# Kernel optimization log

Hardware: AMD Instinct MI355X
Metric: run time of the kernel (lower is better)

## Reference

```python
import jax, jax.numpy as jnp
import numpy as np

HID = 64; D_INNER = 128; D_STATE = 16; DT_RANK = 4; GROUP = 3

def _ln(x, g, b, eps=1e-5):
    m = x.mean(-1, keepdims=True)
    v = ((x - m) ** 2).mean(-1, keepdims=True)
    return (x - m) * jax.lax.rsqrt(v + eps) * g + b

def _conv1x1(x, w, b):
    # x: (B,C,H,W), w: (O,C)
    return jnp.einsum('bchw,oc->bohw', x, w) + b[None, :, None, None]

def _pixel_exchange(F):
    # F: (3,B,C,H,W); vectorized row- then column-exchange with group_size==num_features==3
    _, B, C, H, W = F.shape
    rows = jnp.arange(H); cols = jnp.arange(W)
    R = []
    for d in range(GROUP):
        idx = (d + rows % GROUP) % GROUP  # source feature per row
        R.append(jnp.transpose(F[idx, :, :, rows, :], (1, 2, 0, 3)))
    Rs = jnp.stack(R)
    out = []
    for d in range(GROUP):
        jdx = (d + cols % GROUP) % GROUP  # source feature per column
        out.append(jnp.transpose(Rs[jdx, :, :, :, cols], (1, 2, 3, 0)))
    return out

def _selective_scan(xs, dts, Bs, Cs, A, D):
    # xs,dts: (B,4,d,L); Bs,Cs: (B,4,N,L); A: (4,d,N); D: (4,d)
    xs_t = jnp.moveaxis(xs, -1, 0); dts_t = jnp.moveaxis(dts, -1, 0)
    Bs_t = jnp.moveaxis(Bs, -1, 0); Cs_t = jnp.moveaxis(Cs, -1, 0)
    h0 = jnp.zeros((xs.shape[0], 4, D_INNER, D_STATE), xs.dtype)
    def step(h, inp):
        x_t, dt_t, B_t, C_t = inp
        dA = jnp.exp(dt_t[..., None] * A)
        h = dA * h + (dt_t * x_t)[..., None] * B_t[:, :, None, :]
        y = jnp.einsum('bkdn,bkn->bkd', h, C_t)
        return h, y
    _, ys = jax.lax.scan(step, h0, (xs_t, dts_t, Bs_t, Cs_t))
    ys = jnp.moveaxis(ys, 0, -1)  # (B,4,d,L)
    return ys + D[None, :, :, None] * xs

def _ss2d(x, in_w, in_b, conv_w, conv_b, xproj_w, dt_w, dt_b, A_log, Ds, onorm_g, onorm_b, out_w, out_b):
    B, H, W, C = x.shape; L = H * W
    xz = x @ in_w.T + in_b
    xc, z = xz[..., :D_INNER], xz[..., D_INNER:]
    xc = jnp.transpose(xc, (0, 3, 1, 2))  # (B,d,H,W)
    xc = jax.lax.conv_general_dilated(xc, conv_w, (1, 1), 'SAME',
        dimension_numbers=('NCHW', 'OIHW', 'NCHW'), feature_group_count=D_INNER) + conv_b[None, :, None, None]
    xc = jax.nn.silu(xc)
    x_hw = xc.reshape(B, D_INNER, L)
    x_wh = jnp.transpose(xc, (0, 1, 3, 2)).reshape(B, D_INNER, L)
    xs = jnp.stack([x_hw, x_wh, jnp.flip(x_hw, -1), jnp.flip(x_wh, -1)], axis=1)  # (B,4,d,L)
    x_dbl = jnp.einsum('bkdl,kcd->bkcl', xs, xproj_w)
    dts = jnp.einsum('bkrl,kdr->bkdl', x_dbl[:, :, :DT_RANK], dt_w) + dt_b[None, :, :, None]
    dts = jax.nn.softplus(dts)
    Bs = x_dbl[:, :, DT_RANK:DT_RANK + D_STATE]
    Cs = x_dbl[:, :, DT_RANK + D_STATE:]
    A = -jnp.exp(A_log)
    ys = _selective_scan(xs, dts, Bs, Cs, A, Ds)
    wh2hw = lambda y: jnp.transpose(y.reshape(B, D_INNER, W, H), (0, 1, 3, 2)).reshape(B, D_INNER, L)
    y = ys[:, 0] + jnp.flip(ys[:, 2], -1) + wh2hw(ys[:, 1]) + wh2hw(jnp.flip(ys[:, 3], -1))
    y = _ln(jnp.transpose(y, (0, 2, 1)), onorm_g, onorm_b)  # (B,L,d)
    y = y * jax.nn.silu(z.reshape(B, L, D_INNER))
    return (y @ out_w.T + out_b).reshape(B, H, W, HID)

def _vss(x, p):
    return x + _ss2d(_ln(x, p[0], p[1]), *p[2:])

def reference(x1, x2, x3, aw1, ab1, aw2, ab2, aw3, ab3, ln_g, ln_b, in_w, in_b, conv_w, conv_b, xproj_w, dt_w, dt_b, A_log, Ds, onorm_g, onorm_b, out_w, out_b, k1_w, k1_b, k2_w, k2_b, q3_w, q3_b, v3_w, v3_b, proj_w, proj_b, bn_g, bn_b):
    feats = jnp.stack([_conv1x1(x1, aw1, ab1), _conv1x1(x2, aw2, ab2), _conv1x1(x3, aw3, ab3)])
    ex = _pixel_exchange(feats)
    vss_out = []
    for i in range(3):
        p = (ln_g[i], ln_b[i], in_w[i], in_b[i], conv_w[i], conv_b[i], xproj_w[i], dt_w[i], dt_b[i], A_log[i], Ds[i], onorm_g[i], onorm_b[i], out_w[i], out_b[i])
        xin = jnp.transpose(ex[i], (0, 2, 3, 1))
        vss_out.append(jnp.transpose(_vss(xin, p), (0, 3, 1, 2)))
    v1, v2, v3 = vss_out
    B, C, H, W = v1.shape; L = H * W
    K1 = _conv1x1(v1, k1_w, k1_b).reshape(B, C, L)
    K2 = _conv1x1(v2, k2_w, k2_b).reshape(B, C, L)
    Q = jnp.transpose(_conv1x1(v3, q3_w, q3_b).reshape(B, C, L), (0, 2, 1))
    V = jnp.transpose(_conv1x1(v3, v3_w, v3_b).reshape(B, C, L), (0, 2, 1))
    scale = 1.0 / jnp.sqrt(jnp.asarray(C, jnp.float32))
    a1 = jax.nn.softmax(jnp.einsum('blc,bcm->blm', Q, K1) * scale, axis=-1)
    O1 = jnp.einsum('blm,bmc->blc', a1, V)
    a2 = jax.nn.softmax(jnp.einsum('blc,bcm->blm', Q, K2) * scale, axis=-1)
    O2 = jnp.einsum('blm,bmc->blc', a2, V)
    fused = jnp.transpose(O1 + O2, (0, 2, 1)).reshape(B, C, H, W)
    cat = jnp.concatenate([fused, v1, v2], axis=1)
    out = _conv1x1(cat, proj_w, proj_b)
    m = out.mean((0, 2, 3), keepdims=True)
    var = ((out - m) ** 2).mean((0, 2, 3), keepdims=True)
    out = (out - m) * jax.lax.rsqrt(var + 1e-5) * bn_g[None, :, None, None] + bn_b[None, :, None, None]
    return jax.nn.relu(out)

def setup_inputs() -> dict:
    key = jax.random.key(0)
    ks = iter(jax.random.split(key, 64))
    nrm = lambda shape, s=0.02: jax.random.normal(next(ks), shape, jnp.float32) * s
    B, H, W = 2, 64, 64
    d = {}
    d['x1'] = jax.random.normal(next(ks), (B, 128, H, W), jnp.float32)
    d['x2'] = jax.random.normal(next(ks), (B, 256, H, W), jnp.float32)
    d['x3'] = jax.random.normal(next(ks), (B, 512, H, W), jnp.float32)
    d['aw1'] = nrm((HID, 128)); d['ab1'] = jnp.zeros((HID,), jnp.float32)
    d['aw2'] = nrm((HID, 256)); d['ab2'] = jnp.zeros((HID,), jnp.float32)
    d['aw3'] = nrm((HID, 512)); d['ab3'] = jnp.zeros((HID,), jnp.float32)
    d['ln_g'] = jnp.ones((3, HID), jnp.float32); d['ln_b'] = jnp.zeros((3, HID), jnp.float32)
    d['in_w'] = nrm((3, 2 * D_INNER, HID)); d['in_b'] = jnp.zeros((3, 2 * D_INNER), jnp.float32)
    d['conv_w'] = nrm((3, D_INNER, 1, 3, 3), 0.1); d['conv_b'] = jnp.zeros((3, D_INNER), jnp.float32)
    d['xproj_w'] = nrm((3, 4, DT_RANK + 2 * D_STATE, D_INNER))
    d['dt_w'] = nrm((3, 4, D_INNER, DT_RANK), 0.1); d['dt_b'] = nrm((3, 4, D_INNER), 0.1)
    d['A_log'] = jnp.log(jnp.broadcast_to(jnp.arange(1, D_STATE + 1, dtype=jnp.float32), (3, 4, D_INNER, D_STATE)))
    d['Ds'] = jnp.ones((3, 4, D_INNER), jnp.float32)
    d['onorm_g'] = jnp.ones((3, D_INNER), jnp.float32); d['onorm_b'] = jnp.zeros((3, D_INNER), jnp.float32)
    d['out_w'] = nrm((3, HID, D_INNER)); d['out_b'] = jnp.zeros((3, HID), jnp.float32)
    for nm in ['k1', 'k2', 'q3', 'v3']:
        d[nm + '_w'] = nrm((HID, HID)); d[nm + '_b'] = jnp.zeros((HID,), jnp.float32)
    d['proj_w'] = nrm((HID, 3 * HID)); d['proj_b'] = jnp.zeros((HID,), jnp.float32)
    d['bn_g'] = jnp.ones((HID,), jnp.float32); d['bn_b'] = jnp.zeros((HID,), jnp.float32)
    return d
```

## Files before the change

kernel.cpp:

```cpp
#include <hip/hip_runtime.h>
#include <math.h>

#define B_   2
#define L_   4096
#define DI_  128
#define NCH  64
#define TCH  64
#define SUB  16
#define RS   68
#define SLICE 2144

static constexpr size_t OFF_XC   = 0;
static constexpr size_t OFF_Y    = 0;
static constexpr size_t OFF_XC2  = 3145728;
static constexpr size_t OFF_XC2T = 6291456;
static constexpr size_t OFF_BC   = 9437184;
static constexpr size_t OFF_SCB  = 12976128;
static constexpr size_t OFF_FE   = 16121856;
static constexpr size_t OFF_Z    = 17694720;
static constexpr size_t OFF_AWT1 = 20840448;
static constexpr size_t OFF_AWT2 = 20848640;
static constexpr size_t OFF_AWT3 = 20865024;
static constexpr size_t OFF_PWT  = 20897792;
static constexpr size_t OFF_DT   = 20910080;
static constexpr size_t OFF_RV   = 27201536;
static constexpr size_t OFF_SS   = 27594752;
static constexpr size_t OFF_VSS  = 3145728;
static constexpr size_t OFF_QB_U  = 0;
static constexpr size_t OFF_K1B_U = 524288;
static constexpr size_t OFF_K2B_U = 1048576;
static constexpr size_t OFF_VB_U  = 1572864;
static constexpr size_t OFF_O1   = 7340032;
static constexpr size_t OFF_O2   = 7864320;
static constexpr size_t OFF_RAW  = 9437184;
static constexpr size_t OFF_ST   = 9961472;
static constexpr size_t OFF_PART = 12976128;

using bf16x8 = __attribute__((ext_vector_type(8))) short;
using f32x4  = __attribute__((ext_vector_type(4))) float;

__device__ inline ushort f2bf(float x) {
    uint u = __float_as_uint(x);
    uint r = (u + 0x7fffu + ((u >> 16) & 1u)) >> 16;
    return (ushort)r;
}
__device__ inline uint pack2(float a, float b) {
    return (uint)f2bf(a) | ((uint)f2bf(b) << 16);
}

#define LOG2E 1.44269504088896340736f

__global__ void __launch_bounds__(256) pex_prep(
    const float* __restrict__ aw1, const float* __restrict__ aw2,
    const float* __restrict__ aw3, const float* __restrict__ pw,
    float* __restrict__ ws)
{
    int idx = blockIdx.x * 256 + threadIdx.x;
    int ic = idx >> 6, c = idx & 63;
    if (ic < 128) ws[OFF_AWT1 + idx] = aw1[c * 128 + ic];
    if (ic < 256) ws[OFF_AWT2 + idx] = aw2[c * 256 + ic];
    ws[OFF_AWT3 + idx] = aw3[c * 512 + ic];
    if (idx < 192 * 64) {
        int cp = idx >> 6;
        ws[OFF_PWT + idx] = pw[c * 192 + cp];
    }
}

__global__ void __launch_bounds__(256) pex_feats(
    const float* __restrict__ x1, const float* __restrict__ x2, const float* __restrict__ x3,
    const float* __restrict__ ab1, const float* __restrict__ ab2, const float* __restrict__ ab3,
    float* __restrict__ ws)
{
    int bid = blockIdx.x;
    int i, base, nk;
    if (bid < 64)       { i = 0; base = 0;   nk = 2; }
    else if (bid < 192) { i = 1; base = 64;  nk = 4; }
    else                { i = 2; base = 192; nk = 8; }
    int r = bid - base;
    int kc = r & (nk - 1);
    int rb = r / nk;
    int b = rb >> 4;
    int p = (rb & 15) * 256 + threadIdx.x;
    int c0 = blockIdx.y * 32;
    const float* xp; const float* ab; const float* awT; int IC;
    if (i == 0)      { xp = x1; ab = ab1; awT = ws + OFF_AWT1; IC = 128; }
    else if (i == 1) { xp = x2; ab = ab2; awT = ws + OFF_AWT2; IC = 256; }
    else             { xp = x3; ab = ab3; awT = ws + OFF_AWT3; IC = 512; }
    (void)IC;
    xp += (size_t)b * IC * L_ + p;
    int ic0 = kc * 64;
    float acc[32];
#pragma unroll
    for (int c = 0; c < 32; ++c) acc[c] = (kc == 0) ? ab[c0 + c] : 0.f;
#pragma unroll 4
    for (int ic = ic0; ic < ic0 + 64; ++ic) {
        float v = xp[(size_t)ic * L_];
        const float4* wr = (const float4*)(awT + ic * 64 + c0);
#pragma unroll
        for (int j = 0; j < 8; ++j) {
            float4 w = wr[j];
            acc[j*4+0] = fmaf(v, w.x, acc[j*4+0]);
            acc[j*4+1] = fmaf(v, w.y, acc[j*4+1]);
            acc[j*4+2] = fmaf(v, w.z, acc[j*4+2]);
            acc[j*4+3] = fmaf(v, w.w, acc[j*4+3]);
        }
    }
    float* fe = ws + OFF_FE + ((size_t)(i * B_ + b) * 64 + c0) * L_ + p;
#pragma unroll
    for (int c = 0; c < 32; ++c) atomicAdd(&fe[(size_t)c * L_], acc[c]);
}

__global__ void __launch_bounds__(256) pex_lnproj(
    const float* __restrict__ lng, const float* __restrict__ lnb,
    const float* __restrict__ inw, const float* __restrict__ inb,
    float* __restrict__ ws)
{
    __shared__ float wsm[32 * 64];
    int bid = blockIdx.x;
    int i = bid >> 5;
    int r = bid & 31;
    int b = r >> 4;
    int p = (r & 15) * 256 + threadIdx.x;
    int oc0 = blockIdx.y * 32;
    const float* wbase = inw + (size_t)i * 256 * 64 + (size_t)oc0 * 64;
#pragma unroll
    for (int j = 0; j < 8; ++j)
        wsm[j * 256 + threadIdx.x] = wbase[j * 256 + threadIdx.x];
    __syncthreads();
    int h = p >> 6, w = p & 63;
    int src = (i + h % 3 + w % 3) % 3;
    const float* fe = ws + OFF_FE + (size_t)(src * B_ + b) * 64 * L_ + p;
    float f[64];
    float s = 0.f;
#pragma unroll
    for (int c = 0; c < 64; ++c) { f[c] = fe[(size_t)c * L_]; s += f[c]; }
    float mean = s * (1.f / 64.f);
    float vs = 0.f;
#pragma unroll
    for (int c = 0; c < 64; ++c) { float d = f[c] - mean; vs = fmaf(d, d, vs); }
    float rs = rsqrtf(vs * (1.f / 64.f) + 1e-5f);
#pragma unroll
    for (int c = 0; c < 64; ++c)
        f[c] = (f[c] - mean) * rs * lng[i * 64 + c] + lnb[i * 64 + c];

    float* outp;
    int od;
    if (oc0 < 128) { outp = ws + OFF_XC + (size_t)(i * B_ + b) * DI_ * L_ + p; od = oc0; }
    else           { outp = ws + OFF_Z  + (size_t)(i * B_ + b) * DI_ * L_ + p; od = oc0 - 128; }
    for (int oc = 0; oc < 32; ++oc) {
        const float4* wr = (const float4*)(wsm + oc * 64);
        float acc = inb[i * 256 + oc0 + oc];
#pragma unroll
        for (int j = 0; j < 16; ++j) {
            float4 w = wr[j];
            acc = fmaf(f[j*4+0], w.x, acc);
            acc = fmaf(f[j*4+1], w.y, acc);
            acc = fmaf(f[j*4+2], w.z, acc);
            acc = fmaf(f[j*4+3], w.w, acc);
        }
        outp[(size_t)(od + oc) * L_] = acc;
    }
}

__global__ void __launch_bounds__(256) pex_conv(
    const float* __restrict__ cw, const float* __restrict__ cb, float* __restrict__ ws)
{
    __shared__ float sm[64 * 65];
    int bid = blockIdx.x;
    int i = bid >> 8;
    int r = bid & 255;
    int b = r >> 7;
    int d = r & 127;
    float wk[9];
#pragma unroll
    for (int j = 0; j < 9; ++j) wk[j] = cw[(size_t)(i * DI_ + d) * 9 + j];
    float bias = cb[i * DI_ + d];
    const float* xin = ws + OFF_XC + ((size_t)(i * B_ + b) * DI_ + d) * L_;
    float* xo  = ws + OFF_XC2  + ((size_t)(i * B_ + b) * DI_ + d) * L_;
    float* xoT = ws + OFF_XC2T + ((size_t)(i * B_ + b) * DI_ + d) * L_;
#pragma unroll
    for (int j = 0; j < 16; ++j) {
        int p = j * 256 + threadIdx.x;
        int h = p >> 6, w = p & 63;
        float acc = bias;
#pragma unroll
        for (int dh = 0; dh < 3; ++dh) {
            int hh = h + dh - 1;
            if (hh < 0 || hh > 63) continue;
#pragma unroll
            for (int dw = 0; dw < 3; ++dw) {
                int ww = w + dw - 1;
                if (ww < 0 || ww > 63) continue;
                acc = fmaf(xin[hh * 64 + ww], wk[dh * 3 + dw], acc);
            }
        }
        float v = acc / (1.f + __expf(-acc));
        xo[p] = v;
        sm[h * 65 + w] = v;
    }
    __syncthreads();
#pragma unroll
    for (int j = 0; j < 16; ++j) {
        int q = j * 256 + threadIdx.x;
        int h = q & 63, w = q >> 6;
        xoT[q] = sm[h * 65 + w];
    }
}

__global__ void __launch_bounds__(256) pex_bct(
    const float* __restrict__ xpw, float* __restrict__ ws)
{
    int bid = blockIdx.x;
    int tt = bid & 15;
    int ibk = bid >> 4;
    int k = ibk & 3;
    int ib = ibk >> 2;
    int i = ib >> 1;
    int t = tt * 256 + threadIdx.x;
    int ks = k & 1;
    int tx = (k >= 2) ? (L_ - 1 - t) : t;
    const float* xb = ws + (ks ? OFF_XC2T : OFF_XC2) + (size_t)ib * DI_ * L_ + tx;
    float xv[DI_];
#pragma unroll
    for (int dd = 0; dd < DI_; ++dd) xv[dd] = xb[(size_t)dd * L_];
    const float* wb = xpw + (size_t)(i * 4 + k) * 36 * DI_;
    float rvals[4];
#pragma unroll
    for (int c = 0; c < 4; ++c) {
        const float4* wr = (const float4*)(wb + c * DI_);
        float acc = 0.f;
#pragma unroll
        for (int j = 0; j < 32; ++j) {
            float4 w = wr[j];
            acc = fmaf(xv[4*j+0], w.x, acc);
            acc = fmaf(xv[4*j+1], w.y, acc);
            acc = fmaf(xv[4*j+2], w.z, acc);
            acc = fmaf(xv[4*j+3], w.w, acc);
        }
        rvals[c] = acc;
    }
    *(float4*)(ws + OFF_RV + ((size_t)ibk * L_ + t) * 4) =
        make_float4(rvals[0], rvals[1], rvals[2], rvals[3]);
    float* out = ws + OFF_BC + (size_t)ibk * L_ * 32 + (size_t)t * 32;
    for (int c = 0; c < 32; ++c) {
        const float4* wr = (const float4*)(wb + (4 + c) * DI_);
        float acc = 0.f;
#pragma unroll
        for (int j = 0; j < 32; ++j) {
            float4 w = wr[j];
            acc = fmaf(xv[4*j+0], w.x, acc);
            acc = fmaf(xv[4*j+1], w.y, acc);
            acc = fmaf(xv[4*j+2], w.z, acc);
            acc = fmaf(xv[4*j+3], w.w, acc);
        }
        out[(c & 15) * 2 + (c >> 4)] = acc;
    }
}

__global__ void __launch_bounds__(256) pex_dtk(
    const float* __restrict__ dtw, const float* __restrict__ dtb,
    float* __restrict__ ws)
{
    size_t idx = (size_t)blockIdx.x * 256 + threadIdx.x;
    int ibk = idx >> 19;
    int rem = idx & 524287;
    int d = rem >> 12;
    int t = rem & 4095;
    int i = ibk >> 3;
    int k = ibk & 3;
    int pidx = (i * 4 + k) * DI_ + d;
    float4 rv = *(const float4*)(ws + OFF_RV + ((size_t)ibk * L_ + t) * 4);
    float4 w = *(const float4*)(dtw + (size_t)pidx * 4);
    float dtr = fmaf(rv.x, w.x, fmaf(rv.y, w.y, fmaf(rv.z, w.z, fmaf(rv.w, w.w, dtb[pidx]))));
    float dt = (dtr > 20.f) ? dtr : __logf(1.f + __expf(dtr));
    ((_Float16*)(ws + OFF_DT))[idx] = (_Float16)dt;
}

__global__ void __launch_bounds__(256) pex_scan1(
    const float* __restrict__ Alog, float* __restrict__ ws)
{
    __shared__ float lds[4 * SLICE];
    int grp = blockIdx.x;
    int w = threadIdx.x >> 6;
    int lane = threadIdx.x & 63;
    int chunk = blockIdx.y * 4 + w;
    int dh = grp & 1;
    int ibk = grp >> 1;
    int k = ibk & 3;
    int ib = ibk >> 2;
    int i = ib >> 1;
    int ks = k & 1;
    bool rev = (k >= 2);
    int pidx = (i * 4 + k) * DI_ + dh * 64 + lane;
    float* sx = lds + w * SLICE;
    _Float16* sdt = (_Float16*)(sx + 16 * RS);
    float* sbc = sx + 16 * RS + 8 * RS;
    float A[16];
#pragma unroll
    for (int n = 0; n < 16; ++n)
        A[n] = -__expf(Alog[(size_t)pidx * 16 + n]) * LOG2E;
    const float* xrow = ws + (ks ? OFF_XC2T : OFF_XC2) + (size_t)ib * DI_ * L_;
    const _Float16* dtrow = (const _Float16*)(ws + OFF_DT) + (size_t)ibk * DI_ * L_;
    const float* bcb = ws + OFF_BC + (size_t)ibk * L_ * 32;
    int t0 = chunk * TCH;
    float h[16];
#pragma unroll
    for (int n = 0; n < 16; ++n) h[n] = 0.f;
    float S = 0.f;
    int tl = lane & 15, dl0 = lane >> 4;
    for (int rnd = 0; rnd < TCH / SUB; ++rnd) {
        int ts = t0 + rnd * SUB;
#pragma unroll
        for (int j = 0; j < 16; ++j) {
            int dl = j * 4 + dl0;
            int gd = dh * 64 + dl;
            int tp = rev ? (L_ - 1 - (ts + tl)) : (ts + tl);
            sx[tl * RS + dl]  = xrow[(size_t)gd * L_ + tp];
            sdt[tl * RS + dl] = dtrow[(size_t)gd * L_ + ts + tl];
        }
        {
            const float4* bsrc = (const float4*)(bcb + (size_t)ts * 32);
            *(float4*)&sbc[lane * 8]     = bsrc[lane * 2];
            *(float4*)&sbc[lane * 8 + 4] = bsrc[lane * 2 + 1];
        }
#pragma unroll 4
        for (int tt = 0; tt < SUB; ++tt) {
            float x = sx[tt * RS + lane];
            float dt = (float)sdt[tt * RS + lane];
            const float* bcp = sbc + tt * 32;
            float u = dt * x;
            S += dt;
#pragma unroll
            for (int n = 0; n < 16; ++n) {
                float dA = exp2f(dt * A[n]);
                h[n] = fmaf(dA, h[n], u * bcp[2 * n]);
            }
        }
    }
    size_t base = ((size_t)grp * NCH + chunk) * 1024;
#pragma unroll
    for (int n = 0; n < 16; ++n) ws[OFF_SCB + base + lane * 16 + n] = h[n];
    ws[OFF_SS + ((size_t)grp * NCH + chunk) * 64 + lane] = S;
}

__global__ void __launch_bounds__(256) pex_scan2(
    const float* __restrict__ Alog, float* __restrict__ ws)
{
    int chain = blockIdx.x * 256 + threadIdx.x;
    int grp = chain >> 10;
    int t10 = chain & 1023;
    int dl = t10 >> 4, n = t10 & 15;
    int dh = grp & 1;
    int ibk = grp >> 1;
    int k = ibk & 3;
    int i = (ibk >> 2) >> 1;
    int d = dh * 64 + dl;
    int pidx = (i * 4 + k) * DI_ + d;
    float A = -__expf(Alog[(size_t)pidx * 16 + n]) * LOG2E;
    float h = 0.f;
    for (int c = 0; c < NCH; ++c) {
        size_t o = ((size_t)grp * NCH + c) * 1024 + dl * 16 + n;
        float S = ws[OFF_SS + ((size_t)grp * NCH + c) * 64 + dl];
        float b = ws[OFF_SCB + o];
        float ap = exp2f(A * S);
        ws[OFF_SCB + o] = h;
        h = fmaf(ap, h, b);
    }
}

__global__ void __launch_bounds__(256) pex_scan3(
    const float* __restrict__ Alog, const float* __restrict__ Dsp,
    float* __restrict__ ws)
{
    __shared__ float lds[4 * SLICE];
    int grp = blockIdx.x;
    int w = threadIdx.x >> 6;
    int lane = threadIdx.x & 63;
    int chunk = blockIdx.y * 4 + w;
    int dh = grp & 1;
    int ibk = grp >> 1;
    int k = ibk & 3;
    int ib = ibk >> 2;
    int i = ib >> 1;
    int ks = k & 1;
    bool rev = (k >= 2);
    int pidx = (i * 4 + k) * DI_ + dh * 64 + lane;
    float* sx = lds + w * SLICE;
    _Float16* sdt = (_Float16*)(sx + 16 * RS);
    float* sbc = sx + 16 * RS + 8 * RS;
    float A[16];
#pragma unroll
    for (int n = 0; n < 16; ++n)
        A[n] = -__expf(Alog[(size_t)pidx * 16 + n]) * LOG2E;
    float Dv = Dsp[pidx];
    const float* xrow = ws + (ks ? OFF_XC2T : OFF_XC2) + (size_t)ib * DI_ * L_;
    const _Float16* dtrow = (const _Float16*)(ws + OFF_DT) + (size_t)ibk * DI_ * L_;
    const float* bcb = ws + OFF_BC + (size_t)ibk * L_ * 32;
    float* yb = ws + OFF_Y + (size_t)ib * L_ * DI_ + dh * 64 + lane;
    int t0 = chunk * TCH;
    size_t base = ((size_t)grp * NCH + chunk) * 1024;
    float h[16];
#pragma unroll
    for (int n = 0; n < 16; ++n) h[n] = ws[OFF_SCB + base + lane * 16 + n];
    int tl = lane & 15, dl0 = lane >> 4;
    for (int rnd = 0; rnd < TCH / SUB; ++rnd) {
        int ts = t0 + rnd * SUB;
#pragma unroll
        for (int j = 0; j < 16; ++j) {
            int dl = j * 4 + dl0;
            int gd = dh * 64 + dl;
            int tp = rev ? (L_ - 1 - (ts + tl)) : (ts + tl);
            sx[tl * RS + dl]  = xrow[(size_t)gd * L_ + tp];
            sdt[tl * RS + dl] = dtrow[(size_t)gd * L_ + ts + tl];
        }
        {
            const float4* bsrc = (const float4*)(bcb + (size_t)ts * 32);
            *(float4*)&sbc[lane * 8]     = bsrc[lane * 2];
            *(float4*)&sbc[lane * 8 + 4] = bsrc[lane * 2 + 1];
        }
#pragma unroll 2
        for (int tt = 0; tt < SUB; ++tt) {
            float x = sx[tt * RS + lane];
            float dt = (float)sdt[tt * RS + lane];
            int t = ts + tt;
            const float* bcp = sbc + tt * 32;
            float u = dt * x;
            float y = Dv * x;
#pragma unroll
            for (int n = 0; n < 16; ++n) {
                float dA = exp2f(dt * A[n]);
                h[n] = fmaf(dA, h[n], u * bcp[2 * n]);
                y = fmaf(h[n], bcp[2 * n + 1], y);
            }
            int tx = rev ? (L_ - 1 - t) : t;
            int l = ks ? (((tx & 63) << 6) | (tx >> 6)) : tx;
            atomicAdd(&yb[(size_t)l * DI_], y);
        }
    }
}

__global__ void __launch_bounds__(256) pex_comb(
    const float* __restrict__ og, const float* __restrict__ ob,
    const float* __restrict__ ow, const float* __restrict__ obias,
    float* __restrict__ ws)
{
    __shared__ float wsm[16 * 128];
    int bid = blockIdx.x;
    int i = bid >> 5;
    int r = bid & 31;
    int b = r >> 4;
    int l = (r & 15) * 256 + threadIdx.x;
    int oc0 = blockIdx.y * 16;
    const float* wb = ow + (size_t)i * 64 * DI_ + (size_t)oc0 * DI_;
#pragma unroll
    for (int j = 0; j < 8; ++j)
        wsm[j * 256 + threadIdx.x] = wb[j * 256 + threadIdx.x];
    __syncthreads();
    int h = l >> 6, w = l & 63;
    int ib = i * B_ + b;
    const float4* yp = (const float4*)(ws + OFF_Y + ((size_t)ib * L_ + l) * DI_);
    float y[128];
    float s = 0.f;
#pragma unroll
    for (int j = 0; j < 32; ++j) {
        float4 a = yp[j];
        y[j*4+0] = a.x; y[j*4+1] = a.y; y[j*4+2] = a.z; y[j*4+3] = a.w;
        s += (a.x + a.y) + (a.z + a.w);
    }
    float mean = s * (1.f / 128.f);
    float vs = 0.f;
#pragma unroll
    for (int dd = 0; dd < 128; ++dd) { float t = y[dd] - mean; vs = fmaf(t, t, vs); }
    float rs = rsqrtf(vs * (1.f / 128.f) + 1e-5f);
    const float* zp = ws + OFF_Z + (size_t)ib * DI_ * L_ + l;
#pragma unroll
    for (int dd = 0; dd < 128; ++dd) {
        float zv = zp[(size_t)dd * L_];
        float sil = zv / (1.f + __expf(-zv));
        y[dd] = ((y[dd] - mean) * rs * og[i * 128 + dd] + ob[i * 128 + dd]) * sil;
    }
    int src = (i + h % 3 + w % 3) % 3;
    const float* fe = ws + OFF_FE + (size_t)(src * B_ + b) * 64 * L_ + l;
    float* vo = ws + OFF_VSS + (size_t)ib * 64 * L_ + l;
    for (int c = 0; c < 16; ++c) {
        const float4* wr = (const float4*)(wsm + c * DI_);
        float acc = obias[i * 64 + oc0 + c];
#pragma unroll
        for (int j = 0; j < 32; ++j) {
            float4 wv = wr[j];
            acc = fmaf(y[j*4+0], wv.x, acc);
            acc = fmaf(y[j*4+1], wv.y, acc);
            acc = fmaf(y[j*4+2], wv.z, acc);
            acc = fmaf(y[j*4+3], wv.w, acc);
        }
        vo[(size_t)(oc0 + c) * L_] = fe[(size_t)(oc0 + c) * L_] + acc;
    }
}

__global__ void __launch_bounds__(256) pex_qkv(
    const float* __restrict__ qw, const float* __restrict__ qb,
    const float* __restrict__ vw, const float* __restrict__ vb,
    const float* __restrict__ k1w, const float* __restrict__ k1b,
    const float* __restrict__ k2w, const float* __restrict__ k2b,
    float* __restrict__ ws)
{
    __shared__ float wsm[32 * 64];
    int which = blockIdx.y >> 1;
    int half = blockIdx.y & 1;
    int bid = blockIdx.x;
    int b = bid >> 4;
    int l = (bid & 15) * 256 + threadIdx.x;
    const float* wsel; const float* bsel;
    if (which == 0)      { wsel = qw;  bsel = qb;  }
    else if (which == 1) { wsel = vw;  bsel = vb;  }
    else if (which == 2) { wsel = k1w; bsel = k1b; }
    else                 { wsel = k2w; bsel = k2b; }
    int oc0 = half * 32;
    const float* wbase = wsel + (size_t)oc0 * 64;
#pragma unroll
    for (int j = 0; j < 8; ++j)
        wsm[j * 256 + threadIdx.x] = wbase[j * 256 + threadIdx.x];
    __syncthreads();
    int isrc = (which <= 1) ? 2 : (which - 2);
    const float* vp = ws + OFF_VSS + (size_t)(isrc * B_ + b) * 64 * L_ + l;
    float f[64];
#pragma unroll
    for (int c = 0; c < 64; ++c) f[c] = vp[(size_t)c * L_];
    ushort* qkvb = (ushort*)(ws + OFF_XC2T);
    if (which == 1) {
        ushort* Vp = qkvb + OFF_VB_U + (size_t)b * 64 * L_ + l;
        for (int c = 0; c < 32; ++c) {
            const float4* wr = (const float4*)(wsm + c * 64);
            float acc = bsel[oc0 + c];
#pragma unroll
            for (int j = 0; j < 16; ++j) {
                float4 w = wr[j];
                acc = fmaf(f[j*4+0], w.x, acc);
                acc = fmaf(f[j*4+1], w.y, acc);
                acc = fmaf(f[j*4+2], w.z, acc);
                acc = fmaf(f[j*4+3], w.w, acc);
            }
            Vp[(size_t)(oc0 + c) * L_] = f2bf(acc);
        }
    } else {
        size_t ou = (which == 0) ? OFF_QB_U : (which == 2) ? OFF_K1B_U : OFF_K2B_U;
        ushort* Kp = qkvb + ou + ((size_t)b * L_ + l) * 64 + oc0;
#pragma unroll
        for (int g = 0; g < 4; ++g) {
            float o[8];
#pragma unroll
            for (int jj = 0; jj < 8; ++jj) {
                int c = g * 8 + jj;
                const float4* wr = (const float4*)(wsm + c * 64);
                float acc = bsel[oc0 + c];
#pragma unroll
                for (int j = 0; j < 16; ++j) {
                    float4 w = wr[j];
                    acc = fmaf(f[j*4+0], w.x, acc);
                    acc = fmaf(f[j*4+1], w.y, acc);
                    acc = fmaf(f[j*4+2], w.z, acc);
                    acc = fmaf(f[j*4+3], w.w, acc);
                }
                o[jj] = acc;
            }
            uint4 u;
            u.x = pack2(o[0], o[1]); u.y = pack2(o[2], o[3]);
            u.z = pack2(o[4], o[5]); u.w = pack2(o[6], o[7]);
            *(uint4*)&Kp[g * 8] = u;
        }
    }
}

__global__ void __launch_bounds__(256) pex_attn(float* __restrict__ ws)
{
    __shared__ ushort Ksm[2][64 * 72];
    __shared__ ushort Vtm[64 * 72];
    __shared__ ushort Psm[4][16 * 72];
    const ushort* qkvb = (const ushort*)(ws + OFF_XC2T);
    int bid = blockIdx.x;
    int split = blockIdx.y;
    int qt = bid & 127;
    int b  = bid >> 7;
    const ushort* Qg  = qkvb + OFF_QB_U  + ((size_t)b * L_ + qt * 32) * 64;
    const ushort* K1g = qkvb + OFF_K1B_U + (size_t)b * L_ * 64;
    const ushort* K2g = qkvb + OFF_K2B_U + (size_t)b * L_ * 64;
    const ushort* Vg  = qkvb + OFF_VB_U  + (size_t)b * 64 * L_;
    int tid = threadIdx.x;
    int w = tid >> 6, l = tid & 63;
    int mp = w >> 1, wsub = w & 1;
    int lg = l >> 4, lr = l & 15;
    bf16x8 qf0 = *(const bf16x8*)&Qg[(size_t)(wsub * 16 + lr) * 64 + lg * 8];
    bf16x8 qf1 = *(const bf16x8*)&Qg[(size_t)(wsub * 16 + lr) * 64 + 32 + lg * 8];
    f32x4 acc[4];
    float mrun[4], lrun[4];
#pragma unroll
    for (int ct = 0; ct < 4; ++ct) acc[ct] = (f32x4){0.f, 0.f, 0.f, 0.f};
#pragma unroll
    for (int j = 0; j < 4; ++j) { mrun[j] = -INFINITY; lrun[j] = 0.f; }
    ushort* Pw = Psm[w];

    for (int kt = split * 16; kt < split * 16 + 16; ++kt) {
        int ko = kt * 64;
        __syncthreads();
#pragma unroll
        for (int cc = 0; cc < 6; ++cc) {
            int c = cc * 256 + tid;
            int buf = c >> 9;
            int row = (c >> 3) & 63;
            int col = (c & 7) * 8;
            const ushort* src;
            ushort* dst;
            if (buf == 0)      { src = &K1g[(size_t)(ko + row) * 64 + col]; dst = &Ksm[0][row * 72 + col]; }
            else if (buf == 1) { src = &K2g[(size_t)(ko + row) * 64 + col]; dst = &Ksm[1][row * 72 + col]; }
            else               { src = &Vg[(size_t)row * L_ + ko + col];    dst = &Vtm[row * 72 + col]; }
            *(uint4*)dst = *(const uint4*)src;
        }
        __syncthreads();
        const ushort* Km = Ksm[mp];
        f32x4 s[4];
#pragma unroll
        for (int nt = 0; nt < 4; ++nt) {
            bf16x8 kf0 = *(const bf16x8*)&Km[(nt * 16 + lr) * 72 + lg * 8];
            bf16x8 kf1 = *(const bf16x8*)&Km[(nt * 16 + lr) * 72 + 32 + lg * 8];
            f32x4 z = (f32x4){0.f, 0.f, 0.f, 0.f};
            z = __builtin_amdgcn_mfma_f32_16x16x32_bf16(qf0, kf0, z, 0, 0, 0);
            z = __builtin_amdgcn_mfma_f32_16x16x32_bf16(qf1, kf1, z, 0, 0, 0);
            s[nt] = z;
        }
#pragma unroll
        for (int j = 0; j < 4; ++j) {
            float mx = fmaxf(fmaxf(s[0][j], s[1][j]), fmaxf(s[2][j], s[3][j])) * 0.125f;
            mx = fmaxf(mx, __shfl_xor(mx, 1));
            mx = fmaxf(mx, __shfl_xor(mx, 2));
            mx = fmaxf(mx, __shfl_xor(mx, 4));
            mx = fmaxf(mx, __shfl_xor(mx, 8));
            float mn = fmaxf(mrun[j], mx);
            float co = __expf(mrun[j] - mn);
            float ts = 0.f;
            float p0 = __expf(fmaf(s[0][j], 0.125f, -mn));
            float p1 = __expf(fmaf(s[1][j], 0.125f, -mn));
            float p2 = __expf(fmaf(s[2][j], 0.125f, -mn));
            float p3 = __expf(fmaf(s[3][j], 0.125f, -mn));
            ts = (p0 + p1) + (p2 + p3);
            ts += __shfl_xor(ts, 1);
            ts += __shfl_xor(ts, 2);
            ts += __shfl_xor(ts, 4);
            ts += __shfl_xor(ts, 8);
            lrun[j] = fmaf(lrun[j], co, ts);
            mrun[j] = mn;
            int rbase = (lg * 4 + j) * 72 + lr;
            Pw[rbase +  0] = f2bf(p0);
            Pw[rbase + 16] = f2bf(p1);
            Pw[rbase + 32] = f2bf(p2);
            Pw[rbase + 48] = f2bf(p3);
#pragma unroll
            for (int ct = 0; ct < 4; ++ct) acc[ct][j] *= co;
        }
        bf16x8 pf0 = *(const bf16x8*)&Pw[lr * 72 + lg * 8];
        bf16x8 pf1 = *(const bf16x8*)&Pw[lr * 72 + 32 + lg * 8];
#pragma unroll
        for (int ct = 0; ct < 4; ++ct) {
            bf16x8 vf0 = *(const bf16x8*)&Vtm[(ct * 16 + lr) * 72 + lg * 8];
            bf16x8 vf1 = *(const bf16x8*)&Vtm[(ct * 16 + lr) * 72 + 32 + lg * 8];
            f32x4 o = acc[ct];
            o = __builtin_amdgcn_mfma_f32_16x16x32_bf16(pf0, vf0, o, 0, 0, 0);
            o = __builtin_amdgcn_mfma_f32_16x16x32_bf16(pf1, vf1, o, 0, 0, 0);
            acc[ct] = o;
        }
    }
#pragma unroll
    for (int j = 0; j < 4; ++j) {
        int q = qt * 32 + wsub * 16 + lg * 4 + j;
        float* pp = ws + OFF_PART + ((((size_t)b * 2 + mp) * 4096 + q) * 4 + split) * 66;
#pragma unroll
        for (int ct = 0; ct < 4; ++ct) pp[ct * 16 + lr] = acc[ct][j];
        if (lr == 0) { pp[64] = mrun[j]; pp[65] = lrun[j]; }
    }
}

__global__ void __launch_bounds__(256) pex_attc(float* __restrict__ ws)
{
    int idx = blockIdx.x * 256 + threadIdx.x;
    int d = idx & 63;
    int rec2 = idx >> 6;
    int q = rec2 & 4095;
    int bmp = rec2 >> 12;
    int b = bmp >> 1, mp = bmp & 1;
    const float* pb = ws + OFF_PART + (size_t)rec2 * 4 * 66;
    float m0 = pb[64],        l0 = pb[65];
    float m1 = pb[66 + 64],   l1 = pb[66 + 65];
    float m2 = pb[132 + 64],  l2 = pb[132 + 65];
    float m3 = pb[198 + 64],  l3 = pb[198 + 65];
    float mm = fmaxf(fmaxf(m0, m1), fmaxf(m2, m3));
    float e0 = __expf(m0 - mm), e1 = __expf(m1 - mm);
    float e2 = __expf(m2 - mm), e3 = __expf(m3 - mm);
    float denom = fmaf(e0, l0, fmaf(e1, l1, fmaf(e2, l2, e3 * l3)));
    float o = fmaf(e0, pb[d], fmaf(e1, pb[66 + d], fmaf(e2, pb[132 + d], e3 * pb[198 + d])));
    ws[(mp ? OFF_O2 : OFF_O1) + ((size_t)b * L_ + q) * 64 + d] = o / denom;
}

__global__ void __launch_bounds__(256) pex_proj(
    const float* __restrict__ pbias, float* __restrict__ ws)
{
    __shared__ float wsm[64 * 64];
    int part = blockIdx.y;
    int bid = blockIdx.x;
    int b = bid >> 4;
    int l = (bid & 15) * 256 + threadIdx.x;
    const float* wb = ws + OFF_PWT + (size_t)part * 64 * 64;
#pragma unroll
    for (int j = 0; j < 16; ++j)
        wsm[j * 256 + threadIdx.x] = wb[j * 256 + threadIdx.x];
    __syncthreads();
    float acc[64];
#pragma unroll
    for (int c = 0; c < 64; ++c) acc[c] = (part == 0) ? pbias[c] : 0.f;
    float v[64];
    if (part == 0) {
        const float4* o1 = (const float4*)(ws + OFF_O1 + ((size_t)b * L_ + l) * 64);
        const float4* o2 = (const float4*)(ws + OFF_O2 + ((size_t)b * L_ + l) * 64);
#pragma unroll
        for (int j = 0; j < 16; ++j) {
            float4 a = o1[j], d = o2[j];
            v[j*4+0] = a.x + d.x; v[j*4+1] = a.y + d.y;
            v[j*4+2] = a.z + d.z; v[j*4+3] = a.w + d.w;
        }
    } else {
        const float* vp = ws + OFF_VSS + (size_t)((part - 1) * B_ + b) * 64 * L_ + l;
#pragma unroll
        for (int c = 0; c < 64; ++c) v[c] = vp[(size_t)c * L_];
    }
    for (int ic = 0; ic < 64; ++ic) {
        const float4* wr = (const float4*)(wsm + ic * 64);
        float vv = v[ic];
#pragma unroll
        for (int u = 0; u < 16; ++u) {
            float4 w = wr[u];
            acc[u*4+0] = fmaf(vv, w.x, acc[u*4+0]);
            acc[u*4+1] = fmaf(vv, w.y, acc[u*4+1]);
            acc[u*4+2] = fmaf(vv, w.z, acc[u*4+2]);
            acc[u*4+3] = fmaf(vv, w.w, acc[u*4+3]);
        }
    }
    float* rp = ws + OFF_RAW + (size_t)b * 64 * L_ + l;
#pragma unroll
    for (int c = 0; c < 64; ++c) atomicAdd(&rp[(size_t)c * L_], acc[c]);
}

__global__ void __launch_bounds__(256) pex_stats(float* __restrict__ ws)
{
    int c = blockIdx.x;
    float s = 0.f, s2 = 0.f;
    for (int idx = threadIdx.x; idx < B_ * L_; idx += 256) {
        int b = idx >> 12;
        int l = idx & 4095;
        float v = ws[OFF_RAW + (size_t)(b * 64 + c) * L_ + l];
        s += v;
        s2 = fmaf(v, v, s2);
    }
    for (int off = 1; off < 64; off <<= 1) {
        s  += __shfl_xor(s, off);
        s2 += __shfl_xor(s2, off);
    }
    __shared__ float ps[8];
    int wid = threadIdx.x >> 6;
    if ((threadIdx.x & 63) == 0) { ps[wid] = s; ps[4 + wid] = s2; }
    __syncthreads();
    if (threadIdx.x == 0) {
        ws[OFF_ST + c]      = ps[0] + ps[1] + ps[2] + ps[3];
        ws[OFF_ST + 64 + c] = ps[4] + ps[5] + ps[6] + ps[7];
    }
}

__global__ void __launch_bounds__(256) pex_bn(
    const float* __restrict__ bng, const float* __restrict__ bnb,
    float* __restrict__ out, const float* __restrict__ ws)
{
    int idx = blockIdx.x * 256 + threadIdx.x;
    int c = (idx >> 12) & 63;
    float sum  = ws[OFF_ST + c];
    float sum2 = ws[OFF_ST + 64 + c];
    float mean = sum * (1.f / 8192.f);
    float var  = sum2 * (1.f / 8192.f) - mean * mean;
    float x = ws[OFF_RAW + idx];
    float y = (x - mean) * rsqrtf(var + 1e-5f) * bng[c] + bnb[c];
    out[idx] = fmaxf(y, 0.f);
}

extern "C" void kernel_launch(void* const* d_in, const int* in_sizes, int n_in,
                              void* d_out, int out_size, void* d_ws, size_t ws_size,
                              hipStream_t stream)
{
    (void)in_sizes; (void)n_in; (void)out_size; (void)ws_size;
    float* ws = (float*)d_ws;
    const float* x1      = (const float*)d_in[0];
    const float* x2      = (const float*)d_in[1];
    const float* x3      = (const float*)d_in[2];
    const float* aw1     = (const float*)d_in[3];
    const float* ab1     = (const float*)d_in[4];
    const float* aw2     = (const float*)d_in[5];
    const float* ab2     = (const float*)d_in[6];
    const float* aw3     = (const float*)d_in[7];
    const float* ab3     = (const float*)d_in[8];
    const float* ln_g    = (const float*)d_in[9];
    const float* ln_b    = (const float*)d_in[10];
    const float* in_w    = (const float*)d_in[11];
    const float* in_b    = (const float*)d_in[12];
    const float* conv_w  = (const float*)d_in[13];
    const float* conv_b  = (const float*)d_in[14];
    const float* xproj_w = (const float*)d_in[15];
    const float* dt_w    = (const float*)d_in[16];
    const float* dt_b    = (const float*)d_in[17];
    const float* A_log   = (const float*)d_in[18];
    const float* Ds      = (const float*)d_in[19];
    const float* onorm_g = (const float*)d_in[20];
    const float* onorm_b = (const float*)d_in[21];
    const float* out_w   = (const float*)d_in[22];
    const float* out_b   = (const float*)d_in[23];
    const float* k1_w    = (const float*)d_in[24];
    const float* k1_b    = (const float*)d_in[25];
    const float* k2_w    = (const float*)d_in[26];
    const float* k2_b    = (const float*)d_in[27];
    const float* q3_w    = (const float*)d_in[28];
    const float* q3_b    = (const float*)d_in[29];
    const float* v3_w    = (const float*)d_in[30];
    const float* v3_b    = (const float*)d_in[31];
    const float* proj_w  = (const float*)d_in[32];
    const float* proj_b  = (const float*)d_in[33];
    const float* bn_g    = (const float*)d_in[34];
    const float* bn_b    = (const float*)d_in[35];

    pex_prep  <<<128, 256, 0, stream>>>(aw1, aw2, aw3, proj_w, ws);
    hipMemsetAsync(ws + OFF_FE, 0, 1572864 * sizeof(float), stream);
    pex_feats <<<dim3(448, 2), 256, 0, stream>>>(x1, x2, x3, ab1, ab2, ab3, ws);
    pex_lnproj<<<dim3(96, 8), 256, 0, stream>>>(ln_g, ln_b, in_w, in_b, ws);
    pex_conv  <<<768, 256, 0, stream>>>(conv_w, conv_b, ws);
    pex_bct   <<<384, 256, 0, stream>>>(xproj_w, ws);
    pex_dtk   <<<49152, 256, 0, stream>>>(dt_w, dt_b, ws);
    hipMemsetAsync(ws + OFF_Y, 0, 3145728 * sizeof(float), stream);
    pex_scan1 <<<dim3(48, NCH / 4), 256, 0, stream>>>(A_log, ws);
    pex_scan2 <<<192, 256, 0, stream>>>(A_log, ws);
    pex_scan3 <<<dim3(48, NCH / 4), 256, 0, stream>>>(A_log, Ds, ws);
    pex_comb  <<<dim3(96, 4), 256, 0, stream>>>(onorm_g, onorm_b, out_w, out_b, ws);
    pex_qkv   <<<dim3(32, 8), 256, 0, stream>>>(q3_w, q3_b, v3_w, v3_b, k1_w, k1_b, k2_w, k2_b, ws);
    hipMemsetAsync(ws + OFF_RAW, 0, 524288 * sizeof(float), stream);
    pex_attn  <<<dim3(256, 4), 256, 0, stream>>>(ws);
    pex_attc  <<<4096, 256, 0, stream>>>(ws);
    pex_proj  <<<dim3(32, 3), 256, 0, stream>>>(proj_b, ws);
    pex_stats <<<64, 256, 0, stream>>>(ws);
    pex_bn    <<<2048, 256, 0, stream>>>(bn_g, bn_b, (float*)d_out, ws);
}
```

Measured before the change: 616.9 us.

## Tile x_proj kernel through shared memory and split output channels across threads

Restructures the x_proj (dt-rank/B/C) kernel. Each block now stages a 64-timestep by 128-channel input tile and the full 36x128 weight matrix in LDS. Each thread computes 9 of the 36 output channels for one timestep, instead of one thread holding 128 inputs in registers and computing all 36 outputs. This removes the heavy register pressure and strided per-thread global loads, and raises the grid from 384 to 1536 blocks for better occupancy. In exchange it uses about 50 KB of LDS per block and writes outputs with scattered per-channel stores.

```diff
diff --git a/kernel.cpp b/kernel.cpp
--- a/kernel.cpp
+++ b/kernel.cpp
@@ -210,50 +210,53 @@
 __global__ void __launch_bounds__(256) pex_bct(
     const float* __restrict__ xpw, float* __restrict__ ws)
 {
+    __shared__ float sxt[128 * 64];
+    __shared__ float wsm[36 * 128];
     int bid = blockIdx.x;
-    int tt = bid & 15;
-    int ibk = bid >> 4;
+    int tt = bid & 63;
+    int ibk = bid >> 6;
     int k = ibk & 3;
     int ib = ibk >> 2;
     int i = ib >> 1;
-    int t = tt * 256 + threadIdx.x;
     int ks = k & 1;
-    int tx = (k >= 2) ? (L_ - 1 - t) : t;
-    const float* xb = ws + (ks ? OFF_XC2T : OFF_XC2) + (size_t)ib * DI_ * L_ + tx;
-    float xv[DI_];
-#pragma unroll
-    for (int dd = 0; dd < DI_; ++dd) xv[dd] = xb[(size_t)dd * L_];
+    bool rev = (k >= 2);
+    int tid = threadIdx.x;
+    int t0 = tt * 64;
     const float* wb = xpw + (size_t)(i * 4 + k) * 36 * DI_;
-    float rvals[4];
-#pragma unroll
-    for (int c = 0; c < 4; ++c) {
-        const float4* wr = (const float4*)(wb + c * DI_);
-        float acc = 0.f;
-#pragma unroll
-        for (int j = 0; j < 32; ++j) {
-            float4 w = wr[j];
-            acc = fmaf(xv[4*j+0], w.x, acc);
-            acc = fmaf(xv[4*j+1], w.y, acc);
-            acc = fmaf(xv[4*j+2], w.z, acc);
-            acc = fmaf(xv[4*j+3], w.w, acc);
-        }
-        rvals[c] = acc;
-    }
-    *(float4*)(ws + OFF_RV + ((size_t)ibk * L_ + t) * 4) =
-        make_float4(rvals[0], rvals[1], rvals[2], rvals[3]);
+    for (int idx = tid; idx < 36 * 128; idx += 256) wsm[idx] = wb[idx];
+    const float* xb = ws + (ks ? OFF_XC2T : OFF_XC2) + (size_t)ib * DI_ * L_;
+#pragma unroll
+    for (int j = 0; j < 32; ++j) {
+        int idx = j * 256 + tid;
+        int ic = idx >> 6, tl2 = idx & 63;
+        int t2 = t0 + tl2;
+        int tx2 = rev ? (L_ - 1 - t2) : t2;
+        sxt[ic * 64 + tl2] = xb[(size_t)ic * L_ + tx2];
+    }
+    __syncthreads();
+    int tl = tid & 63;
+    int cg = tid >> 6;
+    float acc[9];
+#pragma unroll
+    for (int c = 0; c < 9; ++c) acc[c] = 0.f;
+    const float* wg = wsm + cg * 9 * 128;
+    for (int ic = 0; ic < 128; ++ic) {
+        float v = sxt[ic * 64 + tl];
+#pragma unroll
+        for (int c = 0; c < 9; ++c)
+            acc[c] = fmaf(v, wg[c * 128 + ic], acc[c]);
+    }
+    int t = t0 + tl;
+    float* rvp = ws + OFF_RV + ((size_t)ibk * L_ + t) * 4;
     float* out = ws + OFF_BC + (size_t)ibk * L_ * 32 + (size_t)t * 32;
-    for (int c = 0; c < 32; ++c) {
-        const float4* wr = (const float4*)(wb + (4 + c) * DI_);
-        float acc = 0.f;
-#pragma unroll
-        for (int j = 0; j < 32; ++j) {
-            float4 w = wr[j];
-            acc = fmaf(xv[4*j+0], w.x, acc);
-            acc = fmaf(xv[4*j+1], w.y, acc);
-            acc = fmaf(xv[4*j+2], w.z, acc);
-            acc = fmaf(xv[4*j+3], w.w, acc);
-        }
-        out[(c & 15) * 2 + (c >> 4)] = acc;
+#pragma unroll
+    for (int c = 0; c < 9; ++c) {
+        int ca = cg * 9 + c;
+        if (ca < 4) rvp[ca] = acc[c];
+        else {
+            int rbc = ca - 4;
+            out[(rbc & 15) * 2 + (rbc >> 4)] = acc[c];
+        }
     }
 }
 
@@ -835,7 +838,7 @@
     pex_feats <<<dim3(448, 2), 256, 0, stream>>>(x1, x2, x3, ab1, ab2, ab3, ws);
     pex_lnproj<<<dim3(96, 8), 256, 0, stream>>>(ln_g, ln_b, in_w, in_b, ws);
     pex_conv  <<<768, 256, 0, stream>>>(conv_w, conv_b, ws);
-    pex_bct   <<<384, 256, 0, stream>>>(xproj_w, ws);
+    pex_bct   <<<1536, 256, 0, stream>>>(xproj_w, ws);
     pex_dtk   <<<49152, 256, 0, stream>>>(dt_w, dt_b, ws);
     hipMemsetAsync(ws + OFF_Y, 0, 3145728 * sizeof(float), stream);
     pex_scan1 <<<dim3(48, NCH / 4), 256, 0, stream>>>(A_log, ws);
```

Result: faster. 550.8 us (-10.7%).
